# Performance work log

Hardware: AMD Instinct MI355X
Metric: run time of the kernel (lower is better)

## Reference

```python
import jax, jax.numpy as jnp
import numpy as np


def setup_inputs() -> dict:
    key = jax.random.key(0)
    kq, kk, kv = jax.random.split(key, 3)
    B, N, H, D = 1, 4096, 16, 64
    q = jax.random.normal(kq, (B, N, H, D), dtype=jnp.float32)
    k = jax.random.normal(kk, (B, N, H, D), dtype=jnp.float32)
    v = jax.random.normal(kv, (B, N, H, D), dtype=jnp.float32)
    return {"q": q, "k": k, "v": v}


def reference(q, k, v):
    # q, k, v: [b, n, h, d]
    d = q.shape[-1]
    scale = 1.0 / jnp.sqrt(jnp.asarray(d, dtype=q.dtype))
    # scores: [b, h, n_q, n_k]
    scores = jnp.einsum("bqhd,bkhd->bhqk", q, k) * scale
    attn = jax.nn.softmax(scores, axis=-1)
    # output back in [b, n, h, d] layout
    out = jnp.einsum("bhqk,bkhd->bqhd", attn, v)
    return out
```

## Files before the change

### kernel.cpp

```cpp
#include <hip/hip_runtime.h>
#include <hip/hip_bf16.h>

#define H 16
#define D 64
#define NSEQ 4096
#define BM 128
#define BN 64
#define NT (NSEQ / BN)

typedef __attribute__((ext_vector_type(8))) short bf16x8;
typedef __attribute__((ext_vector_type(4))) short short4v;
typedef __attribute__((ext_vector_type(4))) float f32x4;
typedef __attribute__((ext_vector_type(4))) float f4v;

union BF8 { bf16x8 v; unsigned u[4]; };
union S4  { short4v s; unsigned u[2]; };

static __device__ __forceinline__ unsigned pk2(float lo, float hi) {
    __hip_bfloat162 h = __float22bfloat162_rn(float2{lo, hi});
    unsigned u;
    __builtin_memcpy(&u, &h, 4);
    return u;
}

static __device__ __forceinline__ float fexp2(float x) {
#if __has_builtin(__builtin_amdgcn_exp2f)
    return __builtin_amdgcn_exp2f(x);
#else
    return exp2f(x);
#endif
}

#define TO_GBL(p) ((const __attribute__((address_space(1))) int*)(unsigned long long)(p))
#define TO_LDS(p) ((__attribute__((address_space(3))) int*)(unsigned int)(unsigned long long)(p))

__global__ void prep(const float* __restrict__ k, const float* __restrict__ v,
                     short* __restrict__ kb, short* __restrict__ vt) {
    __shared__ short L[64 * 72];
    const int h = blockIdx.y, n0 = blockIdx.x * 64, t = threadIdx.x;
    const int rw = t >> 4, c4 = (t & 15) * 4;
    #pragma unroll
    for (int it = 0; it < 4; ++it) {
        const int row = rw + it * 16;
        const size_t gro = ((size_t)(n0 + row) * H + h) * D + c4;
        f4v kf = *(const f4v*)(k + gro);
        S4 ks;
        ks.u[0] = pk2(kf[0], kf[1]);
        ks.u[1] = pk2(kf[2], kf[3]);
        *(short4v*)(kb + ((size_t)h * NSEQ + n0 + row) * D + c4) = ks.s;

        f4v vf = *(const f4v*)(v + gro);
        S4 vs;
        vs.u[0] = pk2(vf[0], vf[1]);
        vs.u[1] = pk2(vf[2], vf[3]);
        *(short4v*)&L[row * 72 + c4] = vs.s;
    }
    __syncthreads();
    const int tr = t & 15, tc = t >> 4;
    const int r0 = tr * 4, d0 = tc * 4;
    short4v ra[4];
    #pragma unroll
    for (int i = 0; i < 4; ++i) {
        const int s = r0 + i, s32 = s & 31, base32 = (s >> 5) * 32;
        const int phys = base32 + ((s32 >> 3) * 4 + (s32 & 3) + 16 * ((s32 >> 2) & 1));
        ra[i] = *(const short4v*)&L[phys * 72 + d0];
    }
    #pragma unroll
    for (int jj = 0; jj < 4; ++jj) {
        short4v o4 = (short4v){ra[0][jj], ra[1][jj], ra[2][jj], ra[3][jj]};
        *(short4v*)(vt + ((size_t)(h * D + d0 + jj)) * NSEQ + n0 + r0) = o4;
    }
}

__global__ __launch_bounds__(256, 2)
void attn_fwd(const float* __restrict__ q, const short* __restrict__ kb,
              const short* __restrict__ vtb, float* __restrict__ out)
{
    const int h     = blockIdx.y;
    const int qbase = blockIdx.x * BM;
    const int tid   = threadIdx.x;
    const int wave  = tid >> 6;
    const int lane  = tid & 63;
    const int lm    = lane & 15;
    const int quad  = lane >> 4;
    const int sw    = lm & 7;

    __shared__ short Kt[2][BN * D];
    __shared__ short Vt[2][BN * D];

    const float c1 = 0.18033688011112042f;

    bf16x8 bq[2][2];
    #pragma unroll
    for (int g = 0; g < 2; ++g) {
        const int qrow = qbase + wave * 32 + g * 16 + lm;
        #pragma unroll
        for (int kc = 0; kc < 2; ++kc) {
            const float* qp = q + ((size_t)qrow * H + h) * D + kc * 32 + quad * 8;
            f4v q0 = *(const f4v*)qp;
            f4v q1 = *(const f4v*)(qp + 4);
            BF8 b;
            b.u[0] = pk2(q0[0] * c1, q0[1] * c1); b.u[1] = pk2(q0[2] * c1, q0[3] * c1);
            b.u[2] = pk2(q1[0] * c1, q1[1] * c1); b.u[3] = pk2(q1[2] * c1, q1[3] * c1);
            bq[g][kc] = b.v;
        }
    }

    BF8 ones;
    ones.u[0] = ones.u[1] = ones.u[2] = ones.u[3] = 0x3F803F80u;

    const f32x4 fz = (f32x4){0.f, 0.f, 0.f, 0.f};
    f32x4 o[2][4];
    #pragma unroll
    for (int g = 0; g < 2; ++g)
        #pragma unroll
        for (int mb = 0; mb < 4; ++mb) o[g][mb] = fz;
    f32x4 lacc[2];
    lacc[0] = fz; lacc[1] = fz;

    const int ci0 = (wave * 2 + 0) * 64 + lane;
    const int ci1 = (wave * 2 + 1) * 64 + lane;
    const int kr0 = ci0 >> 3, kp0 = (ci0 & 7) ^ (kr0 & 7);
    const int kr1 = ci1 >> 3, kp1 = (ci1 & 7) ^ (kr1 & 7);

    const short* kh = kb  + (size_t)h * NSEQ * D;
    const short* vh = vtb + (size_t)h * D * NSEQ;
    const short* pkA = kh + (size_t)kr0 * D + kp0 * 8;
    const short* pkB = kh + (size_t)kr1 * D + kp1 * 8;
    const short* pvA = vh + (size_t)kr0 * NSEQ + kp0 * 8;
    const short* pvB = vh + (size_t)kr1 * NSEQ + kp1 * 8;

    auto issue = [&](int b) {
        __builtin_amdgcn_global_load_lds(TO_GBL(pkA), TO_LDS(&Kt[b][(wave * 2 + 0) * 512]), 16, 0, 0);
        __builtin_amdgcn_global_load_lds(TO_GBL(pkB), TO_LDS(&Kt[b][(wave * 2 + 1) * 512]), 16, 0, 0);
        __builtin_amdgcn_global_load_lds(TO_GBL(pvA), TO_LDS(&Vt[b][(wave * 2 + 0) * 512]), 16, 0, 0);
        __builtin_amdgcn_global_load_lds(TO_GBL(pvB), TO_LDS(&Vt[b][(wave * 2 + 1) * 512]), 16, 0, 0);
        pkA += BN * D; pkB += BN * D; pvA += BN; pvB += BN;
    };

    const int posK0 = ((0 + quad) ^ sw) * 8;
    const int posK1 = ((4 + quad) ^ sw) * 8;

    auto compute = [&](int b) {
        const short* K_ = Kt[b];
        const short* V_ = Vt[b];
        f32x4 st[2][4];

        #pragma unroll
        for (int nb = 0; nb < 4; ++nb) {
            bf16x8 kf0 = *(const bf16x8*)&K_[(nb * 16 + lm) * 64 + posK0];
            bf16x8 kf1 = *(const bf16x8*)&K_[(nb * 16 + lm) * 64 + posK1];
            #pragma unroll
            for (int g = 0; g < 2; ++g) {
                st[g][nb] = __builtin_amdgcn_mfma_f32_16x16x32_bf16(kf0, bq[g][0], fz, 0, 0, 0);
                st[g][nb] = __builtin_amdgcn_mfma_f32_16x16x32_bf16(kf1, bq[g][1], st[g][nb], 0, 0, 0);
            }
        }

        #pragma unroll
        for (int g = 0; g < 2; ++g)
            #pragma unroll
            for (int nb = 0; nb < 4; ++nb)
                #pragma unroll
                for (int r = 0; r < 4; ++r)
                    st[g][nb][r] = fexp2(st[g][nb][r]);

        BF8 pb[2][2];
        #pragma unroll
        for (int g = 0; g < 2; ++g)
            #pragma unroll
            for (int c = 0; c < 2; ++c) {
                pb[g][c].u[0] = pk2(st[g][2 * c][0],     st[g][2 * c][1]);
                pb[g][c].u[1] = pk2(st[g][2 * c][2],     st[g][2 * c][3]);
                pb[g][c].u[2] = pk2(st[g][2 * c + 1][0], st[g][2 * c + 1][1]);
                pb[g][c].u[3] = pk2(st[g][2 * c + 1][2], st[g][2 * c + 1][3]);
            }

        #pragma unroll
        for (int g = 0; g < 2; ++g) {
            lacc[g] = __builtin_amdgcn_mfma_f32_16x16x32_bf16(ones.v, pb[g][0].v, lacc[g], 0, 0, 0);
            lacc[g] = __builtin_amdgcn_mfma_f32_16x16x32_bf16(ones.v, pb[g][1].v, lacc[g], 0, 0, 0);
        }

        #pragma unroll
        for (int c = 0; c < 2; ++c) {
            const int pos = ((c * 4 + quad) ^ sw) * 8;
            #pragma unroll
            for (int mb = 0; mb < 4; ++mb) {
                bf16x8 vf = *(const bf16x8*)&V_[(mb * 16 + lm) * 64 + pos];
                #pragma unroll
                for (int g = 0; g < 2; ++g)
                    o[g][mb] = __builtin_amdgcn_mfma_f32_16x16x32_bf16(vf, pb[g][c].v, o[g][mb], 0, 0, 0);
            }
        }
    };

    issue(0);

    for (int it = 0; it < NT; it += 2) {
        __syncthreads();
        if (it + 1 < NT) issue(1);
        compute(0);
        __syncthreads();
        if (it + 2 < NT) issue(0);
        compute(1);
    }

    #pragma unroll
    for (int g = 0; g < 2; ++g) {
        const float inv = 1.0f / lacc[g][0];
        const int qrow = qbase + wave * 32 + g * 16 + lm;
        float* op = out + ((size_t)qrow * H + h) * D + quad * 4;
        #pragma unroll
        for (int mb = 0; mb < 4; ++mb) {
            f4v w;
            #pragma unroll
            for (int r = 0; r < 4; ++r) w[r] = o[g][mb][r] * inv;
            *(f4v*)(op + mb * 16) = w;
        }
    }
}

extern "C" void kernel_launch(void* const* d_in, const int* in_sizes, int n_in,
                              void* d_out, int out_size, void* d_ws, size_t ws_size,
                              hipStream_t stream) {
    const float* q = (const float*)d_in[0];
    const float* k = (const float*)d_in[1];
    const float* v = (const float*)d_in[2];
    float* out = (float*)d_out;

    short* kb = (short*)d_ws;
    short* vt = kb + (size_t)H * NSEQ * D;

    prep<<<dim3(NSEQ / 64, H), dim3(256), 0, stream>>>(k, v, kb, vt);
    attn_fwd<<<dim3(NSEQ / BM, H), dim3(256), 0, stream>>>(q, kb, vt, out);
}
```

Before: 166.3 us.

## Split key tile across wave pairs with 512-thread blocks and LDS reduction

Doubles the key tile to 128 and launches 512 threads, so that each pair of waves shares a query group and each wave handles half of the keys in a tile. Partial outputs and row sums are combined through shared memory at the end. This doubles the waves per block and halves the number of loop iterations and barriers per key, aiming for more latency hiding. In exchange it adds a final LDS reduction and doubles LDS per block to 64KB, which may limit how many blocks fit on a CU.

```diff
diff --git a/kernel.cpp b/kernel.cpp
--- a/kernel.cpp
+++ b/kernel.cpp
@@ -5,7 +5,7 @@
 #define D 64
 #define NSEQ 4096
 #define BM 128
-#define BN 64
+#define BN 128
 #define NT (NSEQ / BN)
 
 typedef __attribute__((ext_vector_type(8))) short bf16x8;
@@ -72,10 +72,13 @@
     }
 }
 
-__global__ __launch_bounds__(256, 2)
+__global__ __launch_bounds__(512, 2)
 void attn_fwd(const float* __restrict__ q, const short* __restrict__ kb,
               const short* __restrict__ vtb, float* __restrict__ out)
 {
+    __shared__ short Smem[32768];
+    __shared__ float lsh[128];
+
     const int h     = blockIdx.y;
     const int qbase = blockIdx.x * BM;
     const int tid   = threadIdx.x;
@@ -84,16 +87,15 @@
     const int lm    = lane & 15;
     const int quad  = lane >> 4;
     const int sw    = lm & 7;
-
-    __shared__ short Kt[2][BN * D];
-    __shared__ short Vt[2][BN * D];
+    const int qg    = wave >> 1;
+    const int kh2   = wave & 1;
 
     const float c1 = 0.18033688011112042f;
 
     bf16x8 bq[2][2];
     #pragma unroll
     for (int g = 0; g < 2; ++g) {
-        const int qrow = qbase + wave * 32 + g * 16 + lm;
+        const int qrow = qbase + qg * 32 + g * 16 + lm;
         #pragma unroll
         for (int kc = 0; kc < 2; ++kc) {
             const float* qp = q + ((size_t)qrow * H + h) * D + kc * 32 + quad * 8;
@@ -118,23 +120,27 @@
     f32x4 lacc[2];
     lacc[0] = fz; lacc[1] = fz;
 
-    const int ci0 = (wave * 2 + 0) * 64 + lane;
-    const int ci1 = (wave * 2 + 1) * 64 + lane;
+    const int ci0 = wave * 128 + lane;
+    const int ci1 = ci0 + 64;
     const int kr0 = ci0 >> 3, kp0 = (ci0 & 7) ^ (kr0 & 7);
     const int kr1 = ci1 >> 3, kp1 = (ci1 & 7) ^ (kr1 & 7);
-
-    const short* kh = kb  + (size_t)h * NSEQ * D;
-    const short* vh = vtb + (size_t)h * D * NSEQ;
-    const short* pkA = kh + (size_t)kr0 * D + kp0 * 8;
-    const short* pkB = kh + (size_t)kr1 * D + kp1 * 8;
-    const short* pvA = vh + (size_t)kr0 * NSEQ + kp0 * 8;
-    const short* pvB = vh + (size_t)kr1 * NSEQ + kp1 * 8;
+    const int vr0 = ci0 >> 4, vp0 = ci0 & 15, vc0 = (vp0 & 8) + ((vp0 & 7) ^ (vr0 & 7));
+    const int vr1 = ci1 >> 4, vp1 = ci1 & 15, vc1 = (vp1 & 8) + ((vp1 & 7) ^ (vr1 & 7));
+
+    const short* kh_ = kb  + (size_t)h * NSEQ * D;
+    const short* vh_ = vtb + (size_t)h * D * NSEQ;
+    const short* pkA = kh_ + (size_t)kr0 * D + kp0 * 8;
+    const short* pkB = kh_ + (size_t)kr1 * D + kp1 * 8;
+    const short* pvA = vh_ + (size_t)vr0 * NSEQ + vc0 * 8;
+    const short* pvB = vh_ + (size_t)vr1 * NSEQ + vc1 * 8;
 
     auto issue = [&](int b) {
-        __builtin_amdgcn_global_load_lds(TO_GBL(pkA), TO_LDS(&Kt[b][(wave * 2 + 0) * 512]), 16, 0, 0);
-        __builtin_amdgcn_global_load_lds(TO_GBL(pkB), TO_LDS(&Kt[b][(wave * 2 + 1) * 512]), 16, 0, 0);
-        __builtin_amdgcn_global_load_lds(TO_GBL(pvA), TO_LDS(&Vt[b][(wave * 2 + 0) * 512]), 16, 0, 0);
-        __builtin_amdgcn_global_load_lds(TO_GBL(pvB), TO_LDS(&Vt[b][(wave * 2 + 1) * 512]), 16, 0, 0);
+        short* K_ = Smem + b * 8192;
+        short* V_ = Smem + 16384 + b * 8192;
+        __builtin_amdgcn_global_load_lds(TO_GBL(pkA), TO_LDS(K_ + wave * 1024), 16, 0, 0);
+        __builtin_amdgcn_global_load_lds(TO_GBL(pkB), TO_LDS(K_ + wave * 1024 + 512), 16, 0, 0);
+        __builtin_amdgcn_global_load_lds(TO_GBL(pvA), TO_LDS(V_ + wave * 1024), 16, 0, 0);
+        __builtin_amdgcn_global_load_lds(TO_GBL(pvB), TO_LDS(V_ + wave * 1024 + 512), 16, 0, 0);
         pkA += BN * D; pkB += BN * D; pvA += BN; pvB += BN;
     };
 
@@ -142,14 +148,15 @@
     const int posK1 = ((4 + quad) ^ sw) * 8;
 
     auto compute = [&](int b) {
-        const short* K_ = Kt[b];
-        const short* V_ = Vt[b];
+        const short* K_ = Smem + b * 8192;
+        const short* V_ = Smem + 16384 + b * 8192;
         f32x4 st[2][4];
 
         #pragma unroll
         for (int nb = 0; nb < 4; ++nb) {
-            bf16x8 kf0 = *(const bf16x8*)&K_[(nb * 16 + lm) * 64 + posK0];
-            bf16x8 kf1 = *(const bf16x8*)&K_[(nb * 16 + lm) * 64 + posK1];
+            const int krow = (kh2 * 64 + nb * 16 + lm) * 64;
+            bf16x8 kf0 = *(const bf16x8*)&K_[krow + posK0];
+            bf16x8 kf1 = *(const bf16x8*)&K_[krow + posK1];
             #pragma unroll
             for (int g = 0; g < 2; ++g) {
                 st[g][nb] = __builtin_amdgcn_mfma_f32_16x16x32_bf16(kf0, bq[g][0], fz, 0, 0, 0);
@@ -184,10 +191,10 @@
 
         #pragma unroll
         for (int c = 0; c < 2; ++c) {
-            const int pos = ((c * 4 + quad) ^ sw) * 8;
+            const int posV = (kh2 * 8 + ((c * 4 + quad) ^ sw)) * 8;
             #pragma unroll
             for (int mb = 0; mb < 4; ++mb) {
-                bf16x8 vf = *(const bf16x8*)&V_[(mb * 16 + lm) * 64 + pos];
+                bf16x8 vf = *(const bf16x8*)&V_[(mb * 16 + lm) * 128 + posV];
                 #pragma unroll
                 for (int g = 0; g < 2; ++g)
                     o[g][mb] = __builtin_amdgcn_mfma_f32_16x16x32_bf16(vf, pb[g][c].v, o[g][mb], 0, 0, 0);
@@ -206,17 +213,33 @@
         compute(1);
     }
 
-    #pragma unroll
-    for (int g = 0; g < 2; ++g) {
-        const float inv = 1.0f / lacc[g][0];
-        const int qrow = qbase + wave * 32 + g * 16 + lm;
-        float* op = out + ((size_t)qrow * H + h) * D + quad * 4;
-        #pragma unroll
-        for (int mb = 0; mb < 4; ++mb) {
-            f4v w;
-            #pragma unroll
-            for (int r = 0; r < 4; ++r) w[r] = o[g][mb][r] * inv;
-            *(f4v*)(op + mb * 16) = w;
+    __syncthreads();
+    float* red = (float*)Smem;
+    if (kh2 == 1) {
+        #pragma unroll
+        for (int g = 0; g < 2; ++g) {
+            const int qo = qg * 2176 + (g * 16 + lm) * 68 + quad * 4;
+            #pragma unroll
+            for (int mb = 0; mb < 4; ++mb)
+                *(f4v*)&red[qo + mb * 16] = o[g][mb];
+            if (quad == 0) lsh[qg * 32 + g * 16 + lm] = lacc[g][0];
+        }
+    }
+    __syncthreads();
+    if (kh2 == 0) {
+        #pragma unroll
+        for (int g = 0; g < 2; ++g) {
+            const float inv = 1.0f / (lacc[g][0] + lsh[qg * 32 + g * 16 + lm]);
+            const int qrow = qbase + qg * 32 + g * 16 + lm;
+            const int qo = qg * 2176 + (g * 16 + lm) * 68 + quad * 4;
+            float* op = out + ((size_t)qrow * H + h) * D + quad * 4;
+            #pragma unroll
+            for (int mb = 0; mb < 4; ++mb) {
+                f4v w = o[g][mb] + *(const f4v*)&red[qo + mb * 16];
+                #pragma unroll
+                for (int r = 0; r < 4; ++r) w[r] *= inv;
+                *(f4v*)(op + mb * 16) = w;
+            }
         }
     }
 }
@@ -233,5 +256,5 @@
     short* vt = kb + (size_t)H * NSEQ * D;
 
     prep<<<dim3(NSEQ / 64, H), dim3(256), 0, stream>>>(k, v, kb, vt);
-    attn_fwd<<<dim3(NSEQ / BM, H), dim3(256), 0, stream>>>(q, kb, vt, out);
-}
+    attn_fwd<<<dim3(NSEQ / BM, H), dim3(512), 0, stream>>>(q, kb, vt, out);
+}
```

New measurement: 170.3 us. +2.4%, slower.
